# Optimization experiments

Hardware: AMD Instinct MI355X
Metric: run time of the kernel (lower is better)

The kernel has to match this reference:

```python
import jax, jax.numpy as jnp
import numpy as np

B, S, E, H = 2, 2048, 1024, 16
Dh = E // H
LN_EPS = 1e-5


def setup_inputs() -> dict:
    key = jax.random.key(0)
    ks = jax.random.split(key, 12)
    std = 1.0 / np.sqrt(E)
    inp = {
        "query": jax.random.normal(ks[0], (B, S, E), jnp.float32),
        "key":   jax.random.normal(ks[1], (B, S, E), jnp.float32),
        "value": jax.random.normal(ks[2], (B, S, E), jnp.float32),
        # True = masked. Causal mask so every row keeps >=1 valid entry.
        "mask": jnp.broadcast_to(jnp.triu(jnp.ones((S, S), bool), k=1), (B, S, S)),
        # per-head QKV projections, stacked: weight [H, Dh, E] (torch Linear layout), bias [H, Dh]
        "Wq_w": jax.random.uniform(ks[3], (H, Dh, E), jnp.float32, -std, std),
        "Wq_b": jax.random.uniform(ks[4], (H, Dh), jnp.float32, -std, std),
        "Wk_w": jax.random.uniform(ks[5], (H, Dh, E), jnp.float32, -std, std),
        "Wk_b": jax.random.uniform(ks[6], (H, Dh), jnp.float32, -std, std),
        "Wv_w": jax.random.uniform(ks[7], (H, Dh, E), jnp.float32, -std, std),
        "Wv_b": jax.random.uniform(ks[8], (H, Dh), jnp.float32, -std, std),
        # output projection [E, E] (torch layout: out = x @ W.T + b)
        "out_w": jax.random.uniform(ks[9], (E, E), jnp.float32, -std, std),
        "out_b": jax.random.uniform(ks[10], (E,), jnp.float32, -std, std),
        "ln_g": jnp.ones((E,), jnp.float32),
        "ln_b": jnp.zeros((E,), jnp.float32),
    }
    return inp


def reference(query, key, value, mask, Wq_w, Wq_b, Wk_w, Wk_b, Wv_w, Wv_b, out_w, out_b, ln_g, ln_b):
    # per-head projections (batched over heads): [B,S,E] x [H,Dh,E] -> [B,H,S,Dh]
    q = jnp.einsum('bse,hde->bhsd', query, Wq_w) + Wq_b[None, :, None, :]
    k = jnp.einsum('bse,hde->bhsd', key,   Wk_w) + Wk_b[None, :, None, :]
    v = jnp.einsum('bse,hde->bhsd', value, Wv_w) + Wv_b[None, :, None, :]
    scale = 1.0 / np.sqrt(Dh).astype(np.float32)
    scores = jnp.einsum('bhsd,bhtd->bhst', q, k) * scale  # [B,H,S,S]
    scores = jnp.where(mask[:, None, :, :], -jnp.inf, scores)
    probs = jax.nn.softmax(scores, axis=-1)  # dropout p=0 (eval)
    ctx = jnp.einsum('bhst,bhtd->bhsd', probs, v)  # [B,H,S,Dh]
    att = ctx.transpose(0, 2, 1, 3).reshape(query.shape[0], query.shape[1], -1)  # concat heads [B,S,E]
    proj = att @ out_w.T + out_b  # dropout p=0
    x = query + proj  # residual
    mu = jnp.mean(x, axis=-1, keepdims=True)
    var = jnp.mean(jnp.square(x - mu), axis=-1, keepdims=True)
    return (x - mu) * jax.lax.rsqrt(var + LN_EPS) * ln_g + ln_b
```

## Files before the change

kernel.cpp:

```cpp
#include <hip/hip_runtime.h>
#include <stdint.h>

#define B_ 2
#define S_ 2048
#define E_ 1024
#define H_ 16
#define DH 64
#define M_TOT (B_*S_)

typedef short s16x8 __attribute__((ext_vector_type(8)));
typedef float f32x4 __attribute__((ext_vector_type(4)));
typedef unsigned int u32;
typedef unsigned short u16;

union V8 { uint4 u; s16x8 v; };

__device__ __forceinline__ u32 fbits(float f){ union{float f;u32 i;}x; x.f=f; return x.i; }
__device__ __forceinline__ u32 prround(float f){ return fbits(f)+0x8000u; }
__device__ __forceinline__ u16 f2bf(float f){ return (u16)(prround(f)>>16); }
__device__ __forceinline__ u32 permpack(u32 hi,u32 lo){ return __builtin_amdgcn_perm(hi,lo,0x07060302u); }
__device__ __forceinline__ uint4 pack8r(const float4 a, const float4 b){
    uint4 p;
    p.x = permpack(prround(a.y),prround(a.x));
    p.y = permpack(prround(a.w),prround(a.z));
    p.z = permpack(prround(b.y),prround(b.x));
    p.w = permpack(prround(b.w),prround(b.z));
    return p;
}
__device__ __forceinline__ float exp2_fast(float x){ float r; asm("v_exp_f32 %0, %1":"=v"(r):"v"(x)); return r; }

typedef const __attribute__((address_space(1))) u32* gas_t;
typedef __attribute__((address_space(3))) u32* las_t;
#define GLDS16(gp, lp) __builtin_amdgcn_global_load_lds((gas_t)(gp), (las_t)(lp), 16, 0, 0)

__global__ __launch_bounds__(256) void cvtw(
    const float* __restrict__ w0, const float* __restrict__ w1, const float* __restrict__ w2,
    u16* __restrict__ dst, int n4)
{
    const int z = blockIdx.y;
    const float* s = (z==0)?w0:(z==1)?w1:w2;
    u16* d = dst + (size_t)z*E_*E_;
    int i = blockIdx.x*256 + threadIdx.x;
    const int stride = gridDim.x*256;
    for (; i<n4; i+=stride){
        float4 v = ((const float4*)s)[i];
        uint2 p;
        p.x = permpack(prround(v.y),prround(v.x));
        p.y = permpack(prround(v.w),prround(v.z));
        ((uint2*)d)[i] = p;
    }
}
__global__ __launch_bounds__(256) void cvt1(
    const float* __restrict__ s, u16* __restrict__ d, int n4)
{
    int i = blockIdx.x*256 + threadIdx.x;
    const int stride = gridDim.x*256;
    for (; i<n4; i+=stride){
        float4 v = ((const float4*)s)[i];
        uint2 p;
        p.x = permpack(prround(v.y),prround(v.x));
        p.y = permpack(prround(v.w),prround(v.z));
        ((uint2*)d)[i] = p;
    }
}

__global__ __launch_bounds__(256) void qkv128(
    const float* __restrict__ xq, const float* __restrict__ xk, const float* __restrict__ xv,
    const u16* __restrict__ Wb,
    const float* __restrict__ bq, const float* __restrict__ bk, const float* __restrict__ bv,
    u16* __restrict__ oq, u16* __restrict__ ok_, u16* __restrict__ ovt)
{
    const int bid = blockIdx.x;
    const int c = bid & 7;
    const int t = bid >> 3;
    const int n = t & 7;
    const int g = ((t >> 3) << 3) + c;
    const int m = g & 31, z = g >> 5;

    const float* X = (z==0)?xq:(z==1)?xk:xv;
    const u16* W = Wb + (size_t)z*E_*E_;
    const float* bia = (z==0)?bq:(z==1)?bk:bv;
    const float scale = (z==0)? 0.125f*1.44269504f : 1.0f;

    __shared__ __align__(16) float As0[128*32];
    __shared__ __align__(16) float As1[128*32];
    __shared__ __align__(16) u16  Bs0[128*32];
    __shared__ __align__(16) u16  Bs1[128*32];

    const int tid = threadIdx.x;
    const int wid = tid>>6, lane = tid&63;
    const int lrow = lane&15, quad = lane>>4;
    const int mb = m*128, nb = n*128;
    const int wm = (wid>>1)*64, wn = (wid&1)*64;
    const int arow = lane>>3, akq = lane&7;
    const int brow = lane>>2, bkq = lane&3;

    f32x4 acc[4][4] = {};
    const float* Xb = X + (size_t)mb*E_;
    const u16*  Wn = W + (size_t)nb*E_;

    auto stage = [&](float* Ad, u16* Bd, int k0){
#pragma unroll
        for (int i=0;i<4;i++){
            const int rb = wid*32 + i*8;
            GLDS16(Xb + (size_t)(rb+arow)*E_ + k0 + ((akq^arow)<<2), Ad + rb*32);
        }
#pragma unroll
        for (int i=0;i<2;i++){
            const int rb = wid*32 + i*16;
            GLDS16(Wn + (size_t)(rb+brow)*E_ + k0 + (bkq<<3), Bd + rb*32);
        }
    };
    auto compute = [&](const float* Ad, const u16* Bd){
        s16x8 af[4], bfr[4];
#pragma unroll
        for (int mi=0;mi<4;mi++){
            const int row = wm+mi*16+lrow;
            const int sw = lrow&7;
            const float4 fa = *(const float4*)&Ad[row*32 + (((quad<<1)   )^sw)*4];
            const float4 fb = *(const float4*)&Ad[row*32 + (((quad<<1)|1 )^sw)*4];
            V8 tt; tt.u = pack8r(fa, fb);
            af[mi] = tt.v;
        }
#pragma unroll
        for (int ci=0;ci<4;ci++)
            bfr[ci] = *(const s16x8*)&Bd[(wn+ci*16+lrow)*32 + quad*8];
#pragma unroll
        for (int mi=0;mi<4;mi++)
#pragma unroll
            for (int ci=0;ci<4;ci++)
                acc[mi][ci] = __builtin_amdgcn_mfma_f32_16x16x32_bf16(af[mi], bfr[ci], acc[mi][ci],0,0,0);
    };

    stage(As0, Bs0, 0);
    for (int k0=0; k0<E_; k0+=64){
        __syncthreads();
        if (k0+32 < E_) stage(As1, Bs1, k0+32);
        compute(As0, Bs0);
        __syncthreads();
        if (k0+64 < E_) stage(As0, Bs0, k0+64);
        compute(As1, Bs1);
    }

    if (z < 2){
        u16* O = (z==0)?oq:ok_;
#pragma unroll
        for (int ci=0;ci<4;ci++){
            const int nn = nb+wn+ci*16+lrow;
            const float bval = bia[nn];
            const int h = nn>>6, d = nn&63;
#pragma unroll
            for (int mi=0;mi<4;mi++){
#pragma unroll
                for (int r=0;r<4;r++){
                    const int mm = mb+wm+mi*16+quad*4+r;
                    const int bb = mm>>11, s = mm&(S_-1);
                    O[(((size_t)(bb*H_+h))*S_+s)*DH + d] = f2bf((acc[mi][ci][r]+bval)*scale);
                }
            }
        }
    } else {
#pragma unroll
        for (int ci=0;ci<4;ci++){
            const int nn = nb+wn+ci*16+lrow;
            const float bval = bia[nn];
            const int h = nn>>6, d = nn&63;
#pragma unroll
            for (int mi=0;mi<4;mi++){
                const int m0 = mb+wm+mi*16+quad*4;
                const int bb = m0>>11, s0 = m0&(S_-1);
                uint2 pk;
                pk.x = permpack(prround(acc[mi][ci][1]+bval), prround(acc[mi][ci][0]+bval));
                pk.y = permpack(prround(acc[mi][ci][3]+bval), prround(acc[mi][ci][2]+bval));
                *(uint2*)&ovt[(((size_t)(bb*H_+h))*DH + d)*S_ + s0] = pk;
            }
        }
    }
}

__global__ __launch_bounds__(256) void attn(
    const u16* __restrict__ q_ws, const u16* __restrict__ k_ws,
    const u16* __restrict__ vt_ws, u16* __restrict__ att)
{
    const int bid = blockIdx.x;
    const int c8 = bid & 7;
    const int t = bid >> 3;
    const int p = t & 15;
    const int bh = ((t >> 4) << 3) + c8;
    const int b = bh>>4, h = bh&15;

    const u16* Qb = q_ws + (size_t)bh*S_*DH;
    const u16* Kb = k_ws + (size_t)bh*S_*DH;
    const u16* VT = vt_ws + (size_t)bh*DH*S_;

    __shared__ __align__(16) u16 Ks0[64*64];
    __shared__ __align__(16) u16 Ks1[64*64];
    __shared__ __align__(16) u16 Vt0[64*64];
    __shared__ __align__(16) u16 Vt1[64*64];
    __shared__ __align__(16) u16 Ps[4][16*64];

    const int tid = threadIdx.x;
    const int wid = tid>>6, lane = tid&63;
    const int lrow = lane&15, quad = lane>>4;
    u16* Pw = Ps[wid];

    const int srw = lane>>3;
    const int scs = lane&7;
    const int sgc = scs ^ srw;

    auto stageKV = [&](u16* Kd, u16* Vd, int t0){
#pragma unroll
        for (int g2=0; g2<2; g2++){
            const int rg = wid*16 + g2*8 + srw;
            GLDS16(Kb + (size_t)(t0+rg)*DH + (sgc<<3), Kd + (wid*16+g2*8)*64);
            GLDS16(VT + (size_t)rg*S_ + t0 + (sgc<<3), Vd + (wid*16+g2*8)*64);
        }
    };

    for (int ph=0; ph<2; ph++){
        const int qi = ph ? (31-p) : p;
        const int qb = qi<<6;

        s16x8 qf[2];
#pragma unroll
        for (int ch=0;ch<2;ch++)
            qf[ch] = *(const s16x8*)&Qb[(size_t)(qb+wid*16+lrow)*DH + ch*32 + quad*8];

        f32x4 o[4] = {};
        float l_lane = 0.f;
        const int qglob = qb + wid*16 + lrow;
        const int ntile = qi + 1;

        auto computeTile = [&](const u16* Kd, const u16* Vd, int t0, bool diag){
            f32x4 st[4] = {};
#pragma unroll
            for (int tt=0;tt<4;tt++){
                const int tr = tt*16+lrow;
#pragma unroll
                for (int ch=0;ch<2;ch++){
                    const int slot = (ch*4+quad) ^ (lrow&7);
                    const s16x8 kf = *(const s16x8*)&Kd[tr*64 + slot*8];
                    st[tt] = __builtin_amdgcn_mfma_f32_16x16x32_bf16(kf, qf[ch], st[tt],0,0,0);
                }
            }
            if (diag){
#pragma unroll
                for (int tt=0;tt<4;tt++){
                    const int tg = t0 + tt*16 + quad*4;
#pragma unroll
                    for (int r=0;r<4;r++)
                        if (tg + r > qglob) st[tt][r] = -1e30f;
                }
            }
#pragma unroll
            for (int tt=0;tt<4;tt++){
                const float p0 = exp2_fast(st[tt][0]);
                const float p1 = exp2_fast(st[tt][1]);
                const float p2 = exp2_fast(st[tt][2]);
                const float p3 = exp2_fast(st[tt][3]);
                l_lane += (p0+p1)+(p2+p3);
                const int tc = tt*2 + (quad>>1);
                const int ts = tc ^ (lrow&7);
                const int a0 = lrow*64 + ts*8 + (quad&1)*4;
                *(u32*)&Pw[a0]   = permpack(prround(p1),prround(p0));
                *(u32*)&Pw[a0+2] = permpack(prround(p3),prround(p2));
            }
            s16x8 pb[2];
#pragma unroll
            for (int ch=0;ch<2;ch++){
                const int slot = (ch*4+quad) ^ (lrow&7);
                pb[ch] = *(const s16x8*)&Pw[lrow*64 + slot*8];
            }
#pragma unroll
            for (int cc=0;cc<4;cc++){
                const int vr = cc*16+lrow;
#pragma unroll
                for (int ch=0;ch<2;ch++){
                    const int slot = (ch*4+quad) ^ (lrow&7);
                    const s16x8 vf = *(const s16x8*)&Vd[vr*64 + slot*8];
                    o[cc] = __builtin_amdgcn_mfma_f32_16x16x32_bf16(vf, pb[ch], o[cc],0,0,0);
                }
            }
        };

        __syncthreads();
        stageKV(Ks0, Vt0, 0);
        for (int ti=0; ; ti+=2){
            __syncthreads();
            if (ti+1 < ntile) stageKV(Ks1, Vt1, (ti+1)<<6);
            computeTile(Ks0, Vt0, ti<<6, ti==ntile-1);
            if (ti+1 >= ntile) break;
            __syncthreads();
            if (ti+2 < ntile) stageKV(Ks0, Vt0, (ti+2)<<6);
            computeTile(Ks1, Vt1, (ti+1)<<6, ti+1==ntile-1);
            if (ti+2 >= ntile) break;
        }

        float s = l_lane;
        s += __shfl_xor(s, 16, 64);
        s += __shfl_xor(s, 32, 64);
        const float rl = 1.0f/s;

#pragma unroll
        for (int cc=0;cc<4;cc++){
            uint2 pk;
            pk.x = permpack(prround(o[cc][1]*rl), prround(o[cc][0]*rl));
            pk.y = permpack(prround(o[cc][3]*rl), prround(o[cc][2]*rl));
            *(uint2*)&att[(size_t)(b*S_ + qglob)*E_ + h*DH + cc*16 + quad*4] = pk;
        }
    }
}

__global__ __launch_bounds__(256) void oproj128(
    const u16* __restrict__ A, const u16* __restrict__ W, const float* __restrict__ bias,
    const float* __restrict__ resid, float* __restrict__ out)
{
    const int bid = blockIdx.x;
    const int c = bid & 7;
    const int t = bid >> 3;
    const int n = t & 15;
    const int m = ((t >> 4) << 3) + c;

    __shared__ __align__(16) u16 As0[128*32];
    __shared__ __align__(16) u16 As1[128*32];
    __shared__ __align__(16) u16 Bs0[64*32];
    __shared__ __align__(16) u16 Bs1[64*32];

    const int tid = threadIdx.x;
    const int wid = tid>>6, lane = tid&63;
    const int lrow = lane&15, quad = lane>>4;
    const int mb = m*128, nb = n*64;
    const int srow = lane>>2, skq = lane&3;

    f32x4 acc[2][4] = {};
    const u16* Ab = A + (size_t)mb*E_;
    const u16* Wn = W + (size_t)nb*E_;

    auto stage = [&](u16* Ad, u16* Bd, int k0){
#pragma unroll
        for (int i=0;i<2;i++){
            const int rb = wid*32 + i*16;
            GLDS16(Ab + (size_t)(rb+srow)*E_ + k0 + (skq<<3), Ad + rb*32);
        }
        GLDS16(Wn + (size_t)(wid*16+srow)*E_ + k0 + (skq<<3), Bd + (wid*16)*32);
    };
    auto compute = [&](const u16* Ad, const u16* Bd){
        s16x8 af[2], bfr[4];
#pragma unroll
        for (int mi=0;mi<2;mi++)
            af[mi] = *(const s16x8*)&Ad[(wid*32+mi*16+lrow)*32 + quad*8];
#pragma unroll
        for (int ci=0;ci<4;ci++)
            bfr[ci] = *(const s16x8*)&Bd[(ci*16+lrow)*32 + quad*8];
#pragma unroll
        for (int mi=0;mi<2;mi++)
#pragma unroll
            for (int ci=0;ci<4;ci++)
                acc[mi][ci] = __builtin_amdgcn_mfma_f32_16x16x32_bf16(af[mi], bfr[ci], acc[mi][ci],0,0,0);
    };

    stage(As0, Bs0, 0);
    for (int k0=0; k0<E_; k0+=64){
        __syncthreads();
        if (k0+32 < E_) stage(As1, Bs1, k0+32);
        compute(As0, Bs0);
        __syncthreads();
        if (k0+64 < E_) stage(As0, Bs0, k0+64);
        compute(As1, Bs1);
    }

#pragma unroll
    for (int ci=0;ci<4;ci++){
        const int nn = nb+ci*16+lrow;
        const float bval = bias[nn];
#pragma unroll
        for (int mi=0;mi<2;mi++){
#pragma unroll
            for (int r=0;r<4;r++){
                const int mm = mb+wid*32+mi*16+quad*4+r;
                out[(size_t)mm*E_+nn] = acc[mi][ci][r] + bval + resid[(size_t)mm*E_+nn];
            }
        }
    }
}

__global__ __launch_bounds__(256) void ln_k(
    const float* __restrict__ xin, const float* __restrict__ lg,
    const float* __restrict__ lb, float* __restrict__ out)
{
    const int row = blockIdx.x;
    const int tid = threadIdx.x;
    const int wid = tid>>6, lane = tid&63;
    const float* xr = xin + (size_t)row*E_;

    float x[4];
    float s = 0.f;
#pragma unroll
    for (int i=0;i<4;i++){ const int e = i*256+tid; x[i] = xr[e]; s += x[i]; }
    __shared__ float red[8];
#pragma unroll
    for (int off=32; off>0; off>>=1) s += __shfl_xor(s, off, 64);
    if (lane==0) red[wid] = s;
    __syncthreads();
    const float mu = (red[0]+red[1]+red[2]+red[3]) * (1.f/E_);

    float v = 0.f;
#pragma unroll
    for (int i=0;i<4;i++){ const float d = x[i]-mu; v += d*d; }
#pragma unroll
    for (int off=32; off>0; off>>=1) v += __shfl_xor(v, off, 64);
    if (lane==0) red[wid+4] = v;
    __syncthreads();
    const float var = (red[4]+red[5]+red[6]+red[7]) * (1.f/E_);
    const float rs = rsqrtf(var + 1e-5f);

#pragma unroll
    for (int i=0;i<4;i++){
        const int e = i*256+tid;
        out[(size_t)row*E_+e] = (x[i]-mu)*rs*lg[e] + lb[e];
    }
}

extern "C" void kernel_launch(void* const* d_in, const int* in_sizes, int n_in,
                              void* d_out, int out_size, void* d_ws, size_t ws_size,
                              hipStream_t stream) {
    const float* q_in = (const float*)d_in[0];
    const float* k_in = (const float*)d_in[1];
    const float* v_in = (const float*)d_in[2];
    const float* wq = (const float*)d_in[4];
    const float* bq = (const float*)d_in[5];
    const float* wk = (const float*)d_in[6];
    const float* bk = (const float*)d_in[7];
    const float* wv = (const float*)d_in[8];
    const float* bv = (const float*)d_in[9];
    const float* ow = (const float*)d_in[10];
    const float* ob = (const float*)d_in[11];
    const float* lg = (const float*)d_in[12];
    const float* lb = (const float*)d_in[13];
    float* out = (float*)d_out;

    char* ws = (char*)d_ws;
    const size_t MB = (size_t)1<<20;
    u16* q_ws  = (u16*)(ws);
    u16* k_ws  = (u16*)(ws +  8*MB);
    u16* vt_ws = (u16*)(ws + 16*MB);
    u16* att   = (u16*)(ws + 24*MB);
    u16* Wbf   = (u16*)(ws + 24*MB);
    u16* owbf  = (u16*)(ws + 16*MB);
    float* proj = (float*)ws;

    cvtw<<<dim3(512,3), 256, 0, stream>>>(wq, wk, wv, Wbf, (E_*E_)/4);
    qkv128<<<dim3(768), 256, 0, stream>>>(
        q_in, k_in, v_in, Wbf, bq, bk, bv, q_ws, k_ws, vt_ws);
    attn<<<dim3(512), 256, 0, stream>>>(q_ws, k_ws, vt_ws, att);
    cvt1<<<dim3(1024), 256, 0, stream>>>(ow, owbf, (E_*E_)/4);
    oproj128<<<dim3(512), 256, 0, stream>>>(att, owbf, ob, q_in, proj);
    ln_k<<<dim3(M_TOT), 256, 0, stream>>>(proj, lg, lb, out);
}
```

Measured before the change: 270.9 us.

## Replace LDS-staged QKV and out-proj GEMMs with direct-global register-tiled MFMA loops

Removes shared-memory double buffering from the QKV and output-projection GEMMs. Each wave now loads A and B fragments straight from global memory into registers, with larger per-wave tiles (128x64 and 64x64), 128-thread blocks and occupancy hints. When the workspace is large enough, it also pre-converts the fp32 activations to bf16 in separate kernels so the GEMM reads half the bytes. The cost is no LDS reuse across waves, uncoalesced 16-byte row-strided global loads that lean on L2, and extra conversion passes over the activations.

```diff
diff --git a/kernel.cpp b/kernel.cpp
--- a/kernel.cpp
+++ b/kernel.cpp
@@ -64,8 +64,9 @@
     }
 }
 
-__global__ __launch_bounds__(256) void qkv128(
-    const float* __restrict__ xq, const float* __restrict__ xk, const float* __restrict__ xv,
+template<bool AF32>
+__global__ __launch_bounds__(128, 2) void qkv_gemm(
+    const void* __restrict__ x0, const void* __restrict__ x1, const void* __restrict__ x2,
     const u16* __restrict__ Wb,
     const float* __restrict__ bq, const float* __restrict__ bk, const float* __restrict__ bv,
     u16* __restrict__ oq, u16* __restrict__ ok_, u16* __restrict__ ovt)
@@ -73,87 +74,60 @@
     const int bid = blockIdx.x;
     const int c = bid & 7;
     const int t = bid >> 3;
-    const int n = t & 7;
-    const int g = ((t >> 3) << 3) + c;
-    const int m = g & 31, z = g >> 5;
-
-    const float* X = (z==0)?xq:(z==1)?xk:xv;
+    const int n = t & 15;
+    const int g = ((t >> 4) << 3) + c;
+    const int m = g & 15, z = g >> 4;
+
+    const void* X = (z==0)?x0:(z==1)?x1:x2;
     const u16* W = Wb + (size_t)z*E_*E_;
     const float* bia = (z==0)?bq:(z==1)?bk:bv;
     const float scale = (z==0)? 0.125f*1.44269504f : 1.0f;
 
-    __shared__ __align__(16) float As0[128*32];
-    __shared__ __align__(16) float As1[128*32];
-    __shared__ __align__(16) u16  Bs0[128*32];
-    __shared__ __align__(16) u16  Bs1[128*32];
-
     const int tid = threadIdx.x;
     const int wid = tid>>6, lane = tid&63;
     const int lrow = lane&15, quad = lane>>4;
-    const int mb = m*128, nb = n*128;
-    const int wm = (wid>>1)*64, wn = (wid&1)*64;
-    const int arow = lane>>3, akq = lane&7;
-    const int brow = lane>>2, bkq = lane&3;
-
-    f32x4 acc[4][4] = {};
-    const float* Xb = X + (size_t)mb*E_;
-    const u16*  Wn = W + (size_t)nb*E_;
-
-    auto stage = [&](float* Ad, u16* Bd, int k0){
-#pragma unroll
-        for (int i=0;i<4;i++){
-            const int rb = wid*32 + i*8;
-            GLDS16(Xb + (size_t)(rb+arow)*E_ + k0 + ((akq^arow)<<2), Ad + rb*32);
-        }
-#pragma unroll
-        for (int i=0;i<2;i++){
-            const int rb = wid*32 + i*16;
-            GLDS16(Wn + (size_t)(rb+brow)*E_ + k0 + (bkq<<3), Bd + rb*32);
-        }
-    };
-    auto compute = [&](const float* Ad, const u16* Bd){
-        s16x8 af[4], bfr[4];
-#pragma unroll
-        for (int mi=0;mi<4;mi++){
-            const int row = wm+mi*16+lrow;
-            const int sw = lrow&7;
-            const float4 fa = *(const float4*)&Ad[row*32 + (((quad<<1)   )^sw)*4];
-            const float4 fb = *(const float4*)&Ad[row*32 + (((quad<<1)|1 )^sw)*4];
-            V8 tt; tt.u = pack8r(fa, fb);
-            af[mi] = tt.v;
-        }
-#pragma unroll
-        for (int ci=0;ci<4;ci++)
-            bfr[ci] = *(const s16x8*)&Bd[(wn+ci*16+lrow)*32 + quad*8];
-#pragma unroll
-        for (int mi=0;mi<4;mi++)
-#pragma unroll
-            for (int ci=0;ci<4;ci++)
-                acc[mi][ci] = __builtin_amdgcn_mfma_f32_16x16x32_bf16(af[mi], bfr[ci], acc[mi][ci],0,0,0);
-    };
-
-    stage(As0, Bs0, 0);
-    for (int k0=0; k0<E_; k0+=64){
-        __syncthreads();
-        if (k0+32 < E_) stage(As1, Bs1, k0+32);
-        compute(As0, Bs0);
-        __syncthreads();
-        if (k0+64 < E_) stage(As0, Bs0, k0+64);
-        compute(As1, Bs1);
+    const int mb = m*256 + wid*128;
+    const int nb = n*64;
+
+    f32x4 acc[8][4] = {};
+
+#pragma unroll 2
+    for (int k0=0; k0<E_; k0+=32){
+        s16x8 af[8];
+#pragma unroll
+        for (int mi=0; mi<8; mi++){
+            const int row = mb + mi*16 + lrow;
+            if constexpr (AF32){
+                const float* p = (const float*)X + (size_t)row*E_ + k0 + quad*8;
+                V8 tt; tt.u = pack8r(*(const float4*)p, *(const float4*)(p+4));
+                af[mi] = tt.v;
+            } else {
+                af[mi] = *(const s16x8*)((const u16*)X + (size_t)row*E_ + k0 + quad*8);
+            }
+        }
+        s16x8 bf[4];
+#pragma unroll
+        for (int ci=0; ci<4; ci++)
+            bf[ci] = *(const s16x8*)&W[(size_t)(nb+ci*16+lrow)*E_ + k0 + quad*8];
+#pragma unroll
+        for (int mi=0; mi<8; mi++)
+#pragma unroll
+            for (int ci=0; ci<4; ci++)
+                acc[mi][ci] = __builtin_amdgcn_mfma_f32_16x16x32_bf16(af[mi], bf[ci], acc[mi][ci],0,0,0);
     }
 
     if (z < 2){
         u16* O = (z==0)?oq:ok_;
 #pragma unroll
         for (int ci=0;ci<4;ci++){
-            const int nn = nb+wn+ci*16+lrow;
+            const int nn = nb+ci*16+lrow;
             const float bval = bia[nn];
             const int h = nn>>6, d = nn&63;
 #pragma unroll
-            for (int mi=0;mi<4;mi++){
+            for (int mi=0;mi<8;mi++){
 #pragma unroll
                 for (int r=0;r<4;r++){
-                    const int mm = mb+wm+mi*16+quad*4+r;
+                    const int mm = mb+mi*16+quad*4+r;
                     const int bb = mm>>11, s = mm&(S_-1);
                     O[(((size_t)(bb*H_+h))*S_+s)*DH + d] = f2bf((acc[mi][ci][r]+bval)*scale);
                 }
@@ -162,12 +136,12 @@
     } else {
 #pragma unroll
         for (int ci=0;ci<4;ci++){
-            const int nn = nb+wn+ci*16+lrow;
+            const int nn = nb+ci*16+lrow;
             const float bval = bia[nn];
             const int h = nn>>6, d = nn&63;
 #pragma unroll
-            for (int mi=0;mi<4;mi++){
-                const int m0 = mb+wm+mi*16+quad*4;
+            for (int mi=0;mi<8;mi++){
+                const int m0 = mb+mi*16+quad*4;
                 const int bb = m0>>11, s0 = m0&(S_-1);
                 uint2 pk;
                 pk.x = permpack(prround(acc[mi][ci][1]+bval), prround(acc[mi][ci][0]+bval));
@@ -311,7 +285,7 @@
     }
 }
 
-__global__ __launch_bounds__(256) void oproj128(
+__global__ __launch_bounds__(128, 2) void oproj(
     const u16* __restrict__ A, const u16* __restrict__ W, const float* __restrict__ bias,
     const float* __restrict__ resid, float* __restrict__ out)
 {
@@ -321,52 +295,29 @@
     const int n = t & 15;
     const int m = ((t >> 4) << 3) + c;
 
-    __shared__ __align__(16) u16 As0[128*32];
-    __shared__ __align__(16) u16 As1[128*32];
-    __shared__ __align__(16) u16 Bs0[64*32];
-    __shared__ __align__(16) u16 Bs1[64*32];
-
     const int tid = threadIdx.x;
     const int wid = tid>>6, lane = tid&63;
     const int lrow = lane&15, quad = lane>>4;
-    const int mb = m*128, nb = n*64;
-    const int srow = lane>>2, skq = lane&3;
-
-    f32x4 acc[2][4] = {};
-    const u16* Ab = A + (size_t)mb*E_;
-    const u16* Wn = W + (size_t)nb*E_;
-
-    auto stage = [&](u16* Ad, u16* Bd, int k0){
-#pragma unroll
-        for (int i=0;i<2;i++){
-            const int rb = wid*32 + i*16;
-            GLDS16(Ab + (size_t)(rb+srow)*E_ + k0 + (skq<<3), Ad + rb*32);
-        }
-        GLDS16(Wn + (size_t)(wid*16+srow)*E_ + k0 + (skq<<3), Bd + (wid*16)*32);
-    };
-    auto compute = [&](const u16* Ad, const u16* Bd){
-        s16x8 af[2], bfr[4];
-#pragma unroll
-        for (int mi=0;mi<2;mi++)
-            af[mi] = *(const s16x8*)&Ad[(wid*32+mi*16+lrow)*32 + quad*8];
-#pragma unroll
-        for (int ci=0;ci<4;ci++)
-            bfr[ci] = *(const s16x8*)&Bd[(ci*16+lrow)*32 + quad*8];
-#pragma unroll
-        for (int mi=0;mi<2;mi++)
-#pragma unroll
-            for (int ci=0;ci<4;ci++)
-                acc[mi][ci] = __builtin_amdgcn_mfma_f32_16x16x32_bf16(af[mi], bfr[ci], acc[mi][ci],0,0,0);
-    };
-
-    stage(As0, Bs0, 0);
-    for (int k0=0; k0<E_; k0+=64){
-        __syncthreads();
-        if (k0+32 < E_) stage(As1, Bs1, k0+32);
-        compute(As0, Bs0);
-        __syncthreads();
-        if (k0+64 < E_) stage(As0, Bs0, k0+64);
-        compute(As1, Bs1);
+    const int mb = m*128 + wid*64;
+    const int nb = n*64;
+
+    f32x4 acc[4][4] = {};
+
+#pragma unroll 2
+    for (int k0=0; k0<E_; k0+=32){
+        s16x8 af[4];
+#pragma unroll
+        for (int mi=0; mi<4; mi++)
+            af[mi] = *(const s16x8*)&A[(size_t)(mb+mi*16+lrow)*E_ + k0 + quad*8];
+        s16x8 bf[4];
+#pragma unroll
+        for (int ci=0; ci<4; ci++)
+            bf[ci] = *(const s16x8*)&W[(size_t)(nb+ci*16+lrow)*E_ + k0 + quad*8];
+#pragma unroll
+        for (int mi=0; mi<4; mi++)
+#pragma unroll
+            for (int ci=0; ci<4; ci++)
+                acc[mi][ci] = __builtin_amdgcn_mfma_f32_16x16x32_bf16(af[mi], bf[ci], acc[mi][ci],0,0,0);
     }
 
 #pragma unroll
@@ -374,10 +325,10 @@
         const int nn = nb+ci*16+lrow;
         const float bval = bias[nn];
 #pragma unroll
-        for (int mi=0;mi<2;mi++){
+        for (int mi=0;mi<4;mi++){
 #pragma unroll
             for (int r=0;r<4;r++){
-                const int mm = mb+wid*32+mi*16+quad*4+r;
+                const int mm = mb+mi*16+quad*4+r;
                 out[(size_t)mm*E_+nn] = acc[mi][ci][r] + bval + resid[(size_t)mm*E_+nn];
             }
         }
@@ -441,19 +392,44 @@
 
     char* ws = (char*)d_ws;
     const size_t MB = (size_t)1<<20;
-    u16* q_ws  = (u16*)(ws);
-    u16* k_ws  = (u16*)(ws +  8*MB);
-    u16* vt_ws = (u16*)(ws + 16*MB);
-    u16* att   = (u16*)(ws + 24*MB);
-    u16* Wbf   = (u16*)(ws + 24*MB);
-    u16* owbf  = (u16*)(ws + 16*MB);
-    float* proj = (float*)ws;
-
-    cvtw<<<dim3(512,3), 256, 0, stream>>>(wq, wk, wv, Wbf, (E_*E_)/4);
-    qkv128<<<dim3(768), 256, 0, stream>>>(
-        q_in, k_in, v_in, Wbf, bq, bk, bv, q_ws, k_ws, vt_ws);
-    attn<<<dim3(512), 256, 0, stream>>>(q_ws, k_ws, vt_ws, att);
-    cvt1<<<dim3(1024), 256, 0, stream>>>(ow, owbf, (E_*E_)/4);
-    oproj128<<<dim3(512), 256, 0, stream>>>(att, owbf, ob, q_in, proj);
-    ln_k<<<dim3(M_TOT), 256, 0, stream>>>(proj, lg, lb, out);
-}
+    const int nX4 = (B_*S_*E_)/4;
+
+    if (ws_size >= 56*MB) {
+        u16* Xbf   = (u16*)(ws);
+        u16* Wbf   = (u16*)(ws + 24*MB);
+        u16* owbf  = (u16*)(ws + 24*MB);
+        u16* q_ws  = (u16*)(ws + 32*MB);
+        u16* k_ws  = (u16*)(ws + 40*MB);
+        u16* vt_ws = (u16*)(ws + 48*MB);
+        u16* att   = (u16*)(ws);
+        float* proj = (float*)(ws + 8*MB);
+
+        cvt1<<<dim3(512), 256, 0, stream>>>(q_in, Xbf,              nX4);
+        cvt1<<<dim3(512), 256, 0, stream>>>(k_in, Xbf + (size_t)B_*S_*E_,   nX4);
+        cvt1<<<dim3(512), 256, 0, stream>>>(v_in, Xbf + (size_t)2*B_*S_*E_, nX4);
+        cvtw<<<dim3(512,3), 256, 0, stream>>>(wq, wk, wv, Wbf, (E_*E_)/4);
+        qkv_gemm<false><<<dim3(768), 128, 0, stream>>>(
+            Xbf, Xbf + (size_t)B_*S_*E_, Xbf + (size_t)2*B_*S_*E_,
+            Wbf, bq, bk, bv, q_ws, k_ws, vt_ws);
+        attn<<<dim3(512), 256, 0, stream>>>(q_ws, k_ws, vt_ws, att);
+        cvt1<<<dim3(512), 256, 0, stream>>>(ow, owbf, (E_*E_)/4);
+        oproj<<<dim3(512), 128, 0, stream>>>(att, owbf, ob, q_in, proj);
+        ln_k<<<dim3(M_TOT), 256, 0, stream>>>(proj, lg, lb, out);
+    } else {
+        u16* q_ws  = (u16*)(ws);
+        u16* k_ws  = (u16*)(ws +  8*MB);
+        u16* vt_ws = (u16*)(ws + 16*MB);
+        u16* att   = (u16*)(ws + 24*MB);
+        u16* Wbf   = (u16*)(ws + 24*MB);
+        u16* owbf  = (u16*)(ws + 16*MB);
+        float* proj = (float*)ws;
+
+        cvtw<<<dim3(512,3), 256, 0, stream>>>(wq, wk, wv, Wbf, (E_*E_)/4);
+        qkv_gemm<true><<<dim3(768), 128, 0, stream>>>(
+            q_in, k_in, v_in, Wbf, bq, bk, bv, q_ws, k_ws, vt_ws);
+        attn<<<dim3(512), 256, 0, stream>>>(q_ws, k_ws, vt_ws, att);
+        cvt1<<<dim3(512), 256, 0, stream>>>(ow, owbf, (E_*E_)/4);
+        oproj<<<dim3(512), 128, 0, stream>>>(att, owbf, ob, q_in, proj);
+        ln_k<<<dim3(M_TOT), 256, 0, stream>>>(proj, lg, lb, out);
+    }
+}
```

New measurement: 308.4 us. +13.8%, slower.
